# Kernel tuning notes

Measured on AMD Instinct MI355X. Metric: run time of the kernel, lower is better.

The kernel has to match this reference:

```python
import jax, jax.numpy as jnp
import numpy as np
import math

N_EMBD = 2048
N_HEAD = 16
HEAD_DIM = N_EMBD // N_HEAD
EPS = 1e-6

def rms_norm(x, w):
    xf = x.astype(jnp.float32)
    n = xf * jax.lax.rsqrt(jnp.mean(xf * xf, axis=-1, keepdims=True) + EPS)
    return n.astype(x.dtype) * w

def rotate_embeddings(x):
    # pairs (a, b) -> (-b, a), interleaved on last dim
    x2 = x.reshape(*x.shape[:-1], -1, 2)
    rot = jnp.stack([-x2[..., 1], x2[..., 0]], axis=-1)
    return rot.reshape(x.shape)

def rope_angles(T, hd, dtype):
    # pos = 10000 ** ((-2*arange(0, hd, 2) - 1) / hd)  (faithful to source)
    i = jnp.arange(0, hd, 2, dtype=jnp.float32)
    pos = jnp.power(10000.0, (-2.0 * i - 1.0) / hd)
    token_seq = jnp.arange(T, dtype=jnp.float32)[:, None] * pos[None, :]  # [T, hd/2]
    ang = jnp.concatenate([token_seq, token_seq], axis=-1)  # [T, hd]
    return ang.astype(dtype)

def setup_inputs() -> dict:
    key = jax.random.key(0)
    k1, k2, k3 = jax.random.split(key, 3)
    B, T, C = 2, 2048, N_EMBD
    x = jax.random.normal(k1, (B, T, C), dtype=jnp.float32)
    s = 1.0 / math.sqrt(C)
    W_qkv = jax.random.normal(k2, (3 * C, C), dtype=jnp.float32) * s
    W_proj = jax.random.normal(k3, (C, C), dtype=jnp.float32) * s
    g_qk = jnp.ones((C,), dtype=jnp.float32)
    return {"x": x, "W_qkv": W_qkv, "W_proj": W_proj, "g_qk": g_qk}

def reference(x, W_qkv, W_proj, g_qk):
    B, T, C = x.shape
    H, hd = N_HEAD, HEAD_DIM
    qkv = x @ W_qkv.T  # [B, T, 3C]
    q, k, v = jnp.split(qkv, 3, axis=-1)
    q = rms_norm(q, g_qk)
    k = rms_norm(k, g_qk)
    # [B, H, T, hd]
    q = q.reshape(B, T, H, hd).transpose(0, 2, 1, 3)
    k = k.reshape(B, T, H, hd).transpose(0, 2, 1, 3)
    v = v.reshape(B, T, H, hd).transpose(0, 2, 1, 3)
    ang = rope_angles(T, hd, x.dtype)  # [T, hd]
    cos, sin = jnp.cos(ang), jnp.sin(ang)
    q = q * cos + rotate_embeddings(q) * sin
    k = k * cos + rotate_embeddings(k) * sin
    scale = 1.0 / math.sqrt(hd)  # muP = False
    att = jnp.einsum('bhqd,bhkd->bhqk', q, k) * scale
    causal = jnp.tril(jnp.ones((T, T), dtype=bool))
    att = jnp.where(causal, att, -jnp.inf)
    att = jax.nn.softmax(att, axis=-1)
    y = jnp.einsum('bhqk,bhkd->bhqd', att, v)
    y = y.transpose(0, 2, 1, 3).reshape(B, T, C)
    return y @ W_proj.T
```

## Files before the change

kernel.cpp:

```cpp
#include <hip/hip_runtime.h>
#include <math.h>

typedef __bf16 bf16x8 __attribute__((ext_vector_type(8)));
typedef float f32x4 __attribute__((ext_vector_type(4)));

__device__ __forceinline__ unsigned short f2bf(float x) {
  unsigned int u = __builtin_bit_cast(unsigned int, x);
  unsigned int r = (u + 0x7fffu + ((u >> 16) & 1u)) >> 16;
  return (unsigned short)r;
}
__device__ __forceinline__ float bf2f(unsigned short u) {
  return __builtin_bit_cast(float, ((unsigned int)u) << 16);
}
__device__ __forceinline__ void async16(const void* g, void* l) {
  __builtin_amdgcn_global_load_lds(
      (const __attribute__((address_space(1))) void*)g,
      (__attribute__((address_space(3))) void*)l, 16, 0, 0);
}

__global__ __launch_bounds__(256) void cvt_bf16_k(const float* __restrict__ in,
                                                  unsigned short* __restrict__ out,
                                                  int n8) {
  const int i = blockIdx.x * 256 + threadIdx.x;
  if (i >= n8) return;
  const float4* p = (const float4*)in + (long)i * 2;
  const float4 v0 = p[0], v1 = p[1];
  alignas(16) unsigned short o[8] = {f2bf(v0.x), f2bf(v0.y), f2bf(v0.z), f2bf(v0.w),
                                     f2bf(v1.x), f2bf(v1.y), f2bf(v1.z), f2bf(v1.w)};
  *(uint4*)(out + (long)i * 8) = *(uint4*)o;
}

__global__ __launch_bounds__(256) void rope_tab(float2* __restrict__ tab) {
  const int id = blockIdx.x * 256 + threadIdx.x;
  const int t = id >> 6, i = id & 63;
  const float kf = 13.287712379549449f / 128.f;
  const float a = (float)t * exp2f(-(4.f * (float)i + 1.f) * kf);
  float s, c;
  sincosf(a, &s, &c);
  tab[id] = make_float2(c, s);
}

__global__ __launch_bounds__(512, 2) void gemm256_qkv(
    const unsigned short* __restrict__ A, const unsigned short* __restrict__ B,
    unsigned short* __restrict__ C, unsigned short* __restrict__ Vt, int K) {
  __shared__ unsigned short As[3][256 * 32];
  __shared__ unsigned short Bs[3][256 * 32];
  const int tid = threadIdx.x;
  const int lane = tid & 63;
  const int w = tid >> 6;
  const int wm = w >> 2, wn = w & 3;
  const int fr = lane & 15, fq = lane >> 4;
  const int nbx = gridDim.x;
  const int nwg = nbx * (int)gridDim.y;
  int bid = (int)blockIdx.y * nbx + (int)blockIdx.x;
  bid = (bid & 7) * (nwg >> 3) + (bid >> 3);
  const long m0 = (long)(bid / nbx) * 256;
  const long n0 = (long)(bid % nbx) * 256;
  const int srow_ = tid >> 2;
  const int scol_ = (tid & 3) * 8;
  auto stgA = [&](int buf, int kt, int r) {
    const int row = r * 128 + srow_;
    const int col = scol_ ^ (((row >> 1) & 3) << 3);
    async16(A + (m0 + row) * (long)K + kt * 32 + col, &As[buf][row * 32 + scol_]);
  };
  auto stgB = [&](int buf, int kt, int r) {
    const int row = r * 128 + srow_;
    const int col = scol_ ^ (((row >> 1) & 3) << 3);
    async16(B + (n0 + row) * (long)K + kt * 32 + col, &Bs[buf][row * 32 + scol_]);
  };
  f32x4 acc[8][4] = {};
  const int NT = K >> 5;
  stgA(0, 0, 0); stgA(0, 0, 1); stgB(0, 0, 0); stgB(0, 0, 1);
  stgA(1, 1, 0); stgA(1, 1, 1); stgB(1, 1, 0); stgB(1, 1, 1);
  asm volatile("s_waitcnt vmcnt(4)" ::: "memory");
  __builtin_amdgcn_s_barrier();
  asm volatile("" ::: "memory");
  int cur = 0, nxt = 2;
  for (int t = 0; t < NT; ++t) {
#pragma unroll
    for (int ih = 0; ih < 2; ++ih) {
      bf16x8 a[4], b[4];
#pragma unroll
      for (int i2 = 0; i2 < 4; i2++) {
        const int row = wm * 128 + (ih * 4 + i2) * 16 + fr;
        a[i2] = *(const bf16x8*)&As[cur][row * 32 +
                                         ((fq * 8) ^ (((row >> 1) & 3) << 3))];
      }
#pragma unroll
      for (int j = 0; j < 4; j++) {
        const int row = wn * 64 + j * 16 + fr;
        b[j] = *(const bf16x8*)&Bs[cur][row * 32 +
                                        ((fq * 8) ^ (((row >> 1) & 3) << 3))];
      }
      if (t + 2 < NT) {
        if (ih == 0) {
          stgA(nxt, t + 2, 0);
          stgA(nxt, t + 2, 1);
        } else {
          stgB(nxt, t + 2, 0);
          stgB(nxt, t + 2, 1);
        }
      }
      if (ih == 1) {
        if (t + 2 < NT)
          asm volatile("s_waitcnt vmcnt(4)" ::: "memory");
        else
          asm volatile("s_waitcnt vmcnt(0)" ::: "memory");
      }
      asm volatile("" ::: "memory");
      __builtin_amdgcn_s_barrier();
      asm volatile("" ::: "memory");
      __builtin_amdgcn_s_setprio(1);
#pragma unroll
      for (int i2 = 0; i2 < 4; i2++)
#pragma unroll
        for (int j = 0; j < 4; j++)
          acc[ih * 4 + i2][j] = __builtin_amdgcn_mfma_f32_16x16x32_bf16(
              a[i2], b[j], acc[ih * 4 + i2][j], 0, 0, 0);
      __builtin_amdgcn_s_setprio(0);
      asm volatile("" ::: "memory");
    }
    __builtin_amdgcn_s_barrier();
    asm volatile("" ::: "memory");
    cur = cur == 2 ? 0 : cur + 1;
    nxt = nxt == 2 ? 0 : nxt + 1;
  }
  if (n0 < 4096) {
#pragma unroll
    for (int i = 0; i < 8; i++)
#pragma unroll
      for (int j = 0; j < 4; j++)
#pragma unroll
        for (int r = 0; r < 4; r++) {
          const long m = m0 + wm * 128 + i * 16 + fq * 4 + r;
          const long n = n0 + wn * 64 + j * 16 + fr;
          C[m * 4096 + n] = f2bf(acc[i][j][r]);
        }
  } else {
#pragma unroll
    for (int i = 0; i < 8; i++)
#pragma unroll
      for (int j = 0; j < 4; j++) {
        const long n = n0 + wn * 64 + j * 16 + fr;
        const long vb = ((m0 >> 11) * 16 + ((n - 4096) >> 7)) * (128L * 2048);
        const int d = (int)(n - 4096) & 127;
        const int tt = ((int)m0 & 2047) + wm * 128 + i * 16 + fq * 4;
        alignas(8) unsigned short o[4] = {f2bf(acc[i][j][0]), f2bf(acc[i][j][1]),
                                          f2bf(acc[i][j][2]), f2bf(acc[i][j][3])};
        *(uint2*)&Vt[vb + (long)d * 2048 + tt] = *(uint2*)o;
      }
  }
}

__global__ __launch_bounds__(256) void gemm128(
    const unsigned short* __restrict__ A, const unsigned short* __restrict__ B,
    float* __restrict__ C, int M, int N, int K) {
  __shared__ unsigned short As[2][128 * 32];
  __shared__ unsigned short Bs[2][128 * 32];
  const int tid = threadIdx.x;
  const int lane = tid & 63;
  const int w = tid >> 6;
  const int wr = w >> 1, wc = w & 1;
  const int fr = lane & 15, fq = lane >> 4;
  const int nbx = gridDim.x;
  const int nwg = nbx * (int)gridDim.y;
  int bid = (int)blockIdx.y * nbx + (int)blockIdx.x;
  bid = (bid & 7) * (nwg >> 3) + (bid >> 3);
  const long m0 = (long)(bid / nbx) * 128;
  const long n0 = (long)(bid % nbx) * 128;
  const int sr = lane >> 2, sc = (lane & 3) * 8;
  f32x4 acc[4][4] = {};
  auto stage = [&](int buf, int k0) {
#pragma unroll
    for (int i = 0; i < 2; i++) {
      const int r = (w * 2 + i) * 16 + sr;
      async16(A + (m0 + r) * (long)K + k0 + sc, &As[buf][(w * 2 + i) * 512]);
      async16(B + (n0 + r) * (long)K + k0 + sc, &Bs[buf][(w * 2 + i) * 512]);
    }
  };
  int cur = 0;
  stage(0, 0);
  for (int k0 = 0; k0 < K; k0 += 32) {
    if (k0 + 32 < K) {
      stage(cur ^ 1, k0 + 32);
      asm volatile("s_waitcnt vmcnt(4)" ::: "memory");
    } else {
      asm volatile("s_waitcnt vmcnt(0)" ::: "memory");
    }
    __builtin_amdgcn_s_barrier();
    asm volatile("" ::: "memory");
    bf16x8 a[4], b[4];
#pragma unroll
    for (int i = 0; i < 4; i++)
      a[i] = *(const bf16x8*)&As[cur][(wr * 64 + i * 16 + fr) * 32 + fq * 8];
#pragma unroll
    for (int j = 0; j < 4; j++)
      b[j] = *(const bf16x8*)&Bs[cur][(wc * 64 + j * 16 + fr) * 32 + fq * 8];
#pragma unroll
    for (int i = 0; i < 4; i++)
#pragma unroll
      for (int j = 0; j < 4; j++)
        acc[i][j] =
            __builtin_amdgcn_mfma_f32_16x16x32_bf16(a[i], b[j], acc[i][j], 0, 0, 0);
    asm volatile("" ::: "memory");
    __builtin_amdgcn_s_barrier();
    asm volatile("" ::: "memory");
    cur ^= 1;
  }
#pragma unroll
  for (int i = 0; i < 4; i++)
#pragma unroll
    for (int j = 0; j < 4; j++)
#pragma unroll
      for (int r = 0; r < 4; r++) {
        const long m = m0 + wr * 64 + i * 16 + fq * 4 + r;
        const long n = n0 + wc * 64 + j * 16 + fr;
        C[m * N + n] = acc[i][j][r];
      }
}

__global__ __launch_bounds__(256) void rms_rope(unsigned short* __restrict__ qkv,
                                                const float* __restrict__ g,
                                                const float2* __restrict__ tab) {
  const int m = blockIdx.x;
  const int t = m & 2047;
  const int tid = threadIdx.x;
  const int lane = tid & 63, w = tid >> 6;
  unsigned short* row = qkv + (long)m * 4096;
  const int base = tid * 8;
  alignas(16) unsigned short qs[8], ks[8];
  *(uint4*)qs = *(const uint4*)(row + base);
  *(uint4*)ks = *(const uint4*)(row + 2048 + base);
  float qv[8], kv[8];
  float sq = 0.f, sk = 0.f;
#pragma unroll
  for (int j = 0; j < 8; j++) {
    qv[j] = bf2f(qs[j]);
    kv[j] = bf2f(ks[j]);
    sq += qv[j] * qv[j];
    sk += kv[j] * kv[j];
  }
#pragma unroll
  for (int off = 1; off < 64; off <<= 1) {
    sq += __shfl_xor(sq, off);
    sk += __shfl_xor(sk, off);
  }
  __shared__ float red[2][4];
  if (lane == 0) {
    red[0][w] = sq;
    red[1][w] = sk;
  }
  __syncthreads();
  sq = red[0][0] + red[0][1] + red[0][2] + red[0][3];
  sk = red[1][0] + red[1][1] + red[1][2] + red[1][3];
  const float rq = rsqrtf(sq * (1.f / 2048.f) + 1e-6f);
  const float rk = rsqrtf(sk * (1.f / 2048.f) + 1e-6f);
  float qn[8], kn[8];
#pragma unroll
  for (int j = 0; j < 8; j++) {
    const float gg = g[base + j];
    qn[j] = qv[j] * rq * gg;
    kn[j] = kv[j] * rk * gg;
  }
  const float2* tp = tab + t * 64 + (base & 63);
  alignas(16) unsigned short qo[8], ko[8];
#pragma unroll
  for (int p = 0; p < 8; p += 2) {
    const float2 cs0 = tp[p];
    const float2 cs1 = tp[p + 1];
    qo[p] = f2bf(qn[p] * cs0.x - qn[p + 1] * cs0.y);
    qo[p + 1] = f2bf(qn[p + 1] * cs1.x + qn[p] * cs1.y);
    ko[p] = f2bf(kn[p] * cs0.x - kn[p + 1] * cs0.y);
    ko[p + 1] = f2bf(kn[p + 1] * cs1.x + kn[p] * cs1.y);
  }
  *(uint4*)(row + base) = *(uint4*)qo;
  *(uint4*)(row + 2048 + base) = *(uint4*)ko;
}

__global__ __launch_bounds__(512, 4) void attn64(
    const unsigned short* __restrict__ QKV, const unsigned short* __restrict__ VT,
    unsigned short* __restrict__ Y) {
  const int bid = blockIdx.x;
  const int r_ = bid & 7, s_ = bid >> 3;
  const int slot = s_ >> 4, jj = s_ & 15;
  const int bh = r_ * 4 + slot;
  const int qt = (jj & 1) ? 15 - (jj >> 1) : (jj >> 1);
  const int b = bh >> 4, h = bh & 15;
  const int tid = threadIdx.x, lane = tid & 63, w = tid >> 6;
  const int fr = lane & 15, fq = lane >> 4;
  __shared__ unsigned short Kl[2][64 * 128];
  __shared__ unsigned short Vl[2][128 * 64];
  __shared__ unsigned short Pl[8][16 * 64];
  char* Pb = (char*)&Pl[w][0];
  const long tokbase = (long)b * 2048;
  const unsigned short* Qp = QKV + tokbase * 4096 + h * 128;
  const unsigned short* Kp = Qp + 2048;
  const unsigned short* Vg = VT + (long)bh * (128 * 2048);
  const int qbase = qt * 128;
  bf16x8 aq[4];
  {
    const unsigned short* qp = Qp + (long)(qbase + w * 16 + fr) * 4096 + fq * 8;
#pragma unroll
    for (int ks = 0; ks < 4; ks++) aq[ks] = *(const bf16x8*)(qp + ks * 32);
  }
  const int kR = tid >> 4, kC = (tid & 15) * 8;
  const int vR = tid >> 3, vC = (tid & 7) * 8;
  auto stage = [&](unsigned short* Kd, unsigned short* Vd, int kt) {
#pragma unroll
    for (int i = 0; i < 2; i++) {
      const int rowK = i * 32 + kR;
      async16(Kp + (long)(kt * 64 + rowK) * 4096 + (kC ^ ((rowK & 7) << 3)),
              Kd + i * 4096 + tid * 8);
      const int rowV = i * 64 + vR;
      async16(Vg + (long)rowV * 2048 + kt * 64 + (vC ^ ((rowV & 7) << 3)),
              Vd + i * 4096 + tid * 8);
    }
  };
  float m_i[4], l_i[4];
#pragma unroll
  for (int r = 0; r < 4; r++) {
    m_i[r] = -1e30f;
    l_i[r] = 0.f;
  }
  f32x4 accO[8] = {};
  const float scale = 0.08838834764831845f;
  const int ktmax = 2 * qt + 1;
  int cur = 0;
  stage(Kl[0], Vl[0], 0);
  for (int kt = 0; kt <= ktmax; kt++) {
    if (kt < ktmax) {
      stage(Kl[cur ^ 1], Vl[cur ^ 1], kt + 1);
      asm volatile("s_waitcnt vmcnt(4)" ::: "memory");
    } else {
      asm volatile("s_waitcnt vmcnt(0)" ::: "memory");
    }
    __builtin_amdgcn_s_barrier();
    asm volatile("" ::: "memory");
    const unsigned short* Kc = Kl[cur];
    const unsigned short* Vc = Vl[cur];
    f32x4 accS[4] = {};
    __builtin_amdgcn_s_setprio(1);
#pragma unroll
    for (int n = 0; n < 4; n++) {
      const int rowK = n * 16 + fr;
#pragma unroll
      for (int ks = 0; ks < 4; ks++) {
        bf16x8 bk =
            *(const bf16x8*)&Kc[rowK * 128 + ((ks * 32 + fq * 8) ^ ((fr & 7) << 3))];
        accS[n] = __builtin_amdgcn_mfma_f32_16x16x32_bf16(aq[ks], bk, accS[n], 0, 0, 0);
      }
    }
    __builtin_amdgcn_s_setprio(0);
    if (kt * 64 + 63 > qbase + w * 16) {
#pragma unroll
      for (int n = 0; n < 4; n++)
#pragma unroll
        for (int r = 0; r < 4; r++) {
          const int key = kt * 64 + n * 16 + fr;
          const int qq = qbase + w * 16 + fq * 4 + r;
          accS[n][r] = (key > qq) ? -1e30f : accS[n][r] * scale;
        }
    } else {
#pragma unroll
      for (int n = 0; n < 4; n++)
#pragma unroll
        for (int r = 0; r < 4; r++) accS[n][r] *= scale;
    }
    float mx[4];
    bool need = false;
#pragma unroll
    for (int r = 0; r < 4; r++) {
      float m = fmaxf(fmaxf(accS[0][r], accS[1][r]), fmaxf(accS[2][r], accS[3][r]));
#pragma unroll
      for (int off = 1; off < 16; off <<= 1) m = fmaxf(m, __shfl_xor(m, off));
      mx[r] = m;
      need |= (m > m_i[r] + 8.f);
    }
    if (__any(need)) {
#pragma unroll
      for (int r = 0; r < 4; r++) {
        const float mnew = fmaxf(m_i[r], mx[r]);
        const float alpha = __expf(m_i[r] - mnew);
        m_i[r] = mnew;
        l_i[r] *= alpha;
#pragma unroll
        for (int ds = 0; ds < 8; ds++) accO[ds][r] *= alpha;
      }
    }
#pragma unroll
    for (int n = 0; n < 4; n++)
#pragma unroll
      for (int r = 0; r < 4; r++) accS[n][r] = __expf(accS[n][r] - m_i[r]);
#pragma unroll
    for (int r = 0; r < 4; r++)
      l_i[r] += accS[0][r] + accS[1][r] + accS[2][r] + accS[3][r];
#pragma unroll
    for (int n = 0; n < 4; n++)
#pragma unroll
      for (int r = 0; r < 4; r++) {
        const int row = fq * 4 + r;
        const int byte = row * 128 + ((n * 32 + fr * 2) ^ ((row & 7) << 4));
        *(unsigned short*)(Pb + byte) = f2bf(accS[n][r]);
      }
    __builtin_amdgcn_s_setprio(1);
#pragma unroll
    for (int ks = 0; ks < 2; ks++) {
      bf16x8 ap =
          *(const bf16x8*)(Pb + fr * 128 + ((ks * 64 + fq * 16) ^ ((fr & 7) << 4)));
#pragma unroll
      for (int ds = 0; ds < 8; ds++) {
        bf16x8 bv = *(const bf16x8*)&Vc[(ds * 16 + fr) * 64 +
                                        ((ks * 32 + fq * 8) ^ ((fr & 7) << 3))];
        accO[ds] = __builtin_amdgcn_mfma_f32_16x16x32_bf16(ap, bv, accO[ds], 0, 0, 0);
      }
    }
    __builtin_amdgcn_s_setprio(0);
    asm volatile("" ::: "memory");
    __builtin_amdgcn_s_barrier();
    asm volatile("" ::: "memory");
    cur ^= 1;
  }
#pragma unroll
  for (int r = 0; r < 4; r++) {
#pragma unroll
    for (int off = 1; off < 16; off <<= 1) l_i[r] += __shfl_xor(l_i[r], off);
    l_i[r] = 1.f / l_i[r];
  }
#pragma unroll
  for (int ds = 0; ds < 8; ds++)
#pragma unroll
    for (int r = 0; r < 4; r++) {
      const long trow = tokbase + qbase + w * 16 + fq * 4 + r;
      Y[trow * 2048 + h * 128 + ds * 16 + fr] = f2bf(accO[ds][r] * l_i[r]);
    }
}

extern "C" void kernel_launch(void* const* d_in, const int* in_sizes, int n_in,
                              void* d_out, int out_size, void* d_ws, size_t ws_size,
                              hipStream_t stream) {
  (void)out_size;
  (void)ws_size;
  const float *x = 0, *Wq = 0, *Wp = 0, *g = 0;
  for (int i = 0; i < n_in; i++) {
    switch (in_sizes[i]) {
      case 8388608: x = (const float*)d_in[i]; break;
      case 12582912: Wq = (const float*)d_in[i]; break;
      case 4194304: Wp = (const float*)d_in[i]; break;
      case 2048: g = (const float*)d_in[i]; break;
    }
  }
  if (!x) x = (const float*)d_in[0];
  if (!Wq) Wq = (const float*)d_in[1];
  if (!Wp) Wp = (const float*)d_in[2];
  if (!g) g = (const float*)d_in[3];
  float* out = (float*)d_out;
  char* ws = (char*)d_ws;
  unsigned short* qkv16 = (unsigned short*)ws;
  unsigned short* VtG = (unsigned short*)(ws + 33554432);
  unsigned short* Y = (unsigned short*)(ws + 50331648);
  unsigned short* xb = Y;
  unsigned short* Wqb = (unsigned short*)(ws + 67108864);
  unsigned short* Wpb = (unsigned short*)(ws + 92274688);
  float2* tab = (float2*)(ws + 100663296);

  cvt_bf16_k<<<4096, 256, 0, stream>>>(x, xb, 1048576);
  cvt_bf16_k<<<6144, 256, 0, stream>>>(Wq, Wqb, 1572864);
  cvt_bf16_k<<<2048, 256, 0, stream>>>(Wp, Wpb, 524288);
  rope_tab<<<512, 256, 0, stream>>>(tab);
  gemm256_qkv<<<dim3(24, 16), 512, 0, stream>>>(xb, Wqb, qkv16, VtG, 2048);
  rms_rope<<<4096, 256, 0, stream>>>(qkv16, g, tab);
  attn64<<<512, 512, 0, stream>>>(qkv16, VtG, Y);
  gemm128<<<dim3(16, 32), 256, 0, stream>>>(Y, Wpb, out, 4096, 2048, 2048);
}
```

Baseline: 438.1 us.

## Switch QKV GEMM to double-buffered LDS pipeline with higher occupancy bound

Replaces the triple-buffered, half-split k-loop of the QKV GEMM with a simpler double-buffered loop that issues the next tile's loads, waits, and then runs all 32 MFMAs per k-step. LDS per block shrinks from 96KB to 64KB, and the launch bound asks for 4 waves per SIMD instead of 2. The intent is to improve latency hiding through occupancy rather than deep prefetch. In exchange, prefetch depth drops to one tile, the wait now sits right before compute, and a tighter register budget (acc alone is 128 VGPRs) could cause spills.

```diff
diff --git a/kernel.cpp b/kernel.cpp
--- a/kernel.cpp
+++ b/kernel.cpp
@@ -40,11 +40,11 @@
   tab[id] = make_float2(c, s);
 }
 
-__global__ __launch_bounds__(512, 2) void gemm256_qkv(
+__global__ __launch_bounds__(512, 4) void gemm256_qkv(
     const unsigned short* __restrict__ A, const unsigned short* __restrict__ B,
     unsigned short* __restrict__ C, unsigned short* __restrict__ Vt, int K) {
-  __shared__ unsigned short As[3][256 * 32];
-  __shared__ unsigned short Bs[3][256 * 32];
+  __shared__ unsigned short As[2][256 * 32];
+  __shared__ unsigned short Bs[2][256 * 32];
   const int tid = threadIdx.x;
   const int lane = tid & 63;
   const int w = tid >> 6;
@@ -58,72 +58,53 @@
   const long n0 = (long)(bid % nbx) * 256;
   const int srow_ = tid >> 2;
   const int scol_ = (tid & 3) * 8;
-  auto stgA = [&](int buf, int kt, int r) {
-    const int row = r * 128 + srow_;
-    const int col = scol_ ^ (((row >> 1) & 3) << 3);
-    async16(A + (m0 + row) * (long)K + kt * 32 + col, &As[buf][row * 32 + scol_]);
-  };
-  auto stgB = [&](int buf, int kt, int r) {
-    const int row = r * 128 + srow_;
-    const int col = scol_ ^ (((row >> 1) & 3) << 3);
-    async16(B + (n0 + row) * (long)K + kt * 32 + col, &Bs[buf][row * 32 + scol_]);
+  auto stage = [&](int buf, int kt) {
+#pragma unroll
+    for (int r = 0; r < 2; r++) {
+      const int row = r * 128 + srow_;
+      const int col = scol_ ^ (((row >> 1) & 3) << 3);
+      async16(A + (m0 + row) * (long)K + kt * 32 + col, &As[buf][row * 32 + scol_]);
+      async16(B + (n0 + row) * (long)K + kt * 32 + col, &Bs[buf][row * 32 + scol_]);
+    }
   };
   f32x4 acc[8][4] = {};
   const int NT = K >> 5;
-  stgA(0, 0, 0); stgA(0, 0, 1); stgB(0, 0, 0); stgB(0, 0, 1);
-  stgA(1, 1, 0); stgA(1, 1, 1); stgB(1, 1, 0); stgB(1, 1, 1);
-  asm volatile("s_waitcnt vmcnt(4)" ::: "memory");
-  __builtin_amdgcn_s_barrier();
-  asm volatile("" ::: "memory");
-  int cur = 0, nxt = 2;
+  int cur = 0;
+  stage(0, 0);
   for (int t = 0; t < NT; ++t) {
-#pragma unroll
-    for (int ih = 0; ih < 2; ++ih) {
-      bf16x8 a[4], b[4];
-#pragma unroll
-      for (int i2 = 0; i2 < 4; i2++) {
-        const int row = wm * 128 + (ih * 4 + i2) * 16 + fr;
-        a[i2] = *(const bf16x8*)&As[cur][row * 32 +
-                                         ((fq * 8) ^ (((row >> 1) & 3) << 3))];
-      }
-#pragma unroll
-      for (int j = 0; j < 4; j++) {
-        const int row = wn * 64 + j * 16 + fr;
-        b[j] = *(const bf16x8*)&Bs[cur][row * 32 +
-                                        ((fq * 8) ^ (((row >> 1) & 3) << 3))];
-      }
-      if (t + 2 < NT) {
-        if (ih == 0) {
-          stgA(nxt, t + 2, 0);
-          stgA(nxt, t + 2, 1);
-        } else {
-          stgB(nxt, t + 2, 0);
-          stgB(nxt, t + 2, 1);
-        }
-      }
-      if (ih == 1) {
-        if (t + 2 < NT)
-          asm volatile("s_waitcnt vmcnt(4)" ::: "memory");
-        else
-          asm volatile("s_waitcnt vmcnt(0)" ::: "memory");
-      }
-      asm volatile("" ::: "memory");
-      __builtin_amdgcn_s_barrier();
-      asm volatile("" ::: "memory");
-      __builtin_amdgcn_s_setprio(1);
-#pragma unroll
-      for (int i2 = 0; i2 < 4; i2++)
-#pragma unroll
-        for (int j = 0; j < 4; j++)
-          acc[ih * 4 + i2][j] = __builtin_amdgcn_mfma_f32_16x16x32_bf16(
-              a[i2], b[j], acc[ih * 4 + i2][j], 0, 0, 0);
-      __builtin_amdgcn_s_setprio(0);
-      asm volatile("" ::: "memory");
-    }
-    __builtin_amdgcn_s_barrier();
-    asm volatile("" ::: "memory");
-    cur = cur == 2 ? 0 : cur + 1;
-    nxt = nxt == 2 ? 0 : nxt + 1;
+    if (t + 1 < NT) {
+      stage(cur ^ 1, t + 1);
+      asm volatile("s_waitcnt vmcnt(4)" ::: "memory");
+    } else {
+      asm volatile("s_waitcnt vmcnt(0)" ::: "memory");
+    }
+    __builtin_amdgcn_s_barrier();
+    asm volatile("" ::: "memory");
+    bf16x8 a[8], b[4];
+#pragma unroll
+    for (int i = 0; i < 8; i++) {
+      const int row = wm * 128 + i * 16 + fr;
+      a[i] = *(const bf16x8*)&As[cur][row * 32 +
+                                      ((fq * 8) ^ (((row >> 1) & 3) << 3))];
+    }
+#pragma unroll
+    for (int j = 0; j < 4; j++) {
+      const int row = wn * 64 + j * 16 + fr;
+      b[j] = *(const bf16x8*)&Bs[cur][row * 32 +
+                                      ((fq * 8) ^ (((row >> 1) & 3) << 3))];
+    }
+    __builtin_amdgcn_s_setprio(1);
+#pragma unroll
+    for (int i = 0; i < 8; i++)
+#pragma unroll
+      for (int j = 0; j < 4; j++)
+        acc[i][j] =
+            __builtin_amdgcn_mfma_f32_16x16x32_bf16(a[i], b[j], acc[i][j], 0, 0, 0);
+    __builtin_amdgcn_s_setprio(0);
+    asm volatile("" ::: "memory");
+    __builtin_amdgcn_s_barrier();
+    asm volatile("" ::: "memory");
+    cur ^= 1;
   }
   if (n0 < 4096) {
 #pragma unroll
```

Result: slower. 1.393 ms (+217.9%).
